# Kernel tuning notes

Hardware: AMD Instinct MI355X
Metric: run time of the kernel (lower is better)

The kernel has to match this reference:

```python
import jax, jax.numpy as jnp
import numpy as np

B, T, C = 8, 2048, 1024
HEAD = 64

def setup_inputs() -> dict:
    key = jax.random.key(0)
    k1, k2 = jax.random.split(key)
    x = jax.random.normal(k1, (B, T, C), dtype=jnp.float32)
    # nn.Linear(dim_embedding, head_size, bias=False) weight: [head_size, dim_embedding]
    W_k = jax.random.normal(k2, (HEAD, C), dtype=jnp.float32) * (C ** -0.5)
    return {"x": x, "W_k": W_k}

def reference(x, W_k):
    # Faithful to source: q, k, v are ALL computed with the `key` projection,
    # and the scale is C**-0.5 (embedding dim), as written in the torch code.
    Bx, Tx, Cx = x.shape
    k = jnp.einsum('btc,hc->bth', x, W_k)   # [B,T,HEAD]
    q = k
    v = k
    scale = Cx ** -0.5
    weight = jnp.einsum('bth,bsh->bts', q, k) * scale  # [B,T,T]
    causal = jnp.tril(jnp.ones((Tx, Tx), dtype=bool))
    weight = jnp.where(causal, weight, -jnp.inf)
    weight = jax.nn.softmax(weight, axis=-1)
    # dropout: eval-mode identity (p=0.2 at train time in the source)
    out = jnp.einsum('bts,bsh->bth', weight, v)  # [B,T,HEAD]
    return out
```

## Files before the change

kernel.cpp:

```cpp
#include <hip/hip_runtime.h>
#include <hip/hip_bf16.h>
#include <math.h>

#define SEQ   2048
#define CDIM  1024
#define HD    64
#define NROW  16384
#define CEXP 0.04508422002778112f

typedef float  f32x4  __attribute__((ext_vector_type(4)));
typedef __bf16 bf16x8 __attribute__((ext_vector_type(8)));
typedef int    i32x4  __attribute__((ext_vector_type(4)));

#define AS1 __attribute__((address_space(1)))
#define AS3 __attribute__((address_space(3)))

static __device__ __forceinline__ unsigned pk2(float a, float b) {
    unsigned ua = __builtin_bit_cast(unsigned, a);
    unsigned ub = __builtin_bit_cast(unsigned, b);
    ua += 0x7fffu + ((ua >> 16) & 1u);
    ub += 0x7fffu + ((ub >> 16) & 1u);
    return (ua >> 16) | (ub & 0xffff0000u);
}

static __device__ __forceinline__ bf16x8 cvt8(f32x4 lo, f32x4 hi) {
    i32x4 w = { (int)pk2(lo[0], lo[1]), (int)pk2(lo[2], lo[3]),
                (int)pk2(hi[0], hi[1]), (int)pk2(hi[2], hi[3]) };
    return __builtin_bit_cast(bf16x8, w);
}

__global__ __launch_bounds__(256) void wconv_kernel(const float* __restrict__ W,
                                                    unsigned* __restrict__ Wb) {
    const int i = blockIdx.x * 256 + threadIdx.x;
    float4 v = *(const float4*)(W + (size_t)i * 4);
    uint2 p = make_uint2(pk2(v.x, v.y), pk2(v.z, v.w));
    *(uint2*)(Wb + (size_t)i * 2) = p;
}

template<int S>
struct XProl {
    static __device__ __forceinline__ void run(f32x4 (&XA)[8], f32x4 (&XB)[8],
                                               unsigned long long xa) {
        constexpr int OFF = S * 128;
        asm volatile("global_load_dwordx4 %0, %2, off offset:%3\n\t"
                     "global_load_dwordx4 %1, %2, off offset:%4"
                     : "=&v"(XA[S]), "=&v"(XB[S])
                     : "v"(xa), "n"(OFF), "n"(OFF + 16)
                     : "memory");
        if constexpr (S + 1 < 8) XProl<S + 1>::run(XA, XB, xa);
    }
};

template<int T>
struct XLoop {
    static __device__ __forceinline__ void run(f32x4 (&XA)[8], f32x4 (&XB)[8],
                                               unsigned long long xa,
                                               const char* const (&wp)[4][2],
                                               f32x4 (&acc)[4]) {
        constexpr int WT = (T < 24) ? 14 : 2 * (31 - T);
        asm volatile("s_waitcnt vmcnt(%0)" :: "n"(WT) : "memory");
        __builtin_amdgcn_sched_barrier(0);
        bf16x8 A = cvt8(XA[T & 7], XB[T & 7]);
        #pragma unroll
        for (int nt = 0; nt < 4; ++nt) {
            bf16x8 B = *(const bf16x8*)(wp[nt][T & 1] + (T >> 1) * 128);
            acc[nt] = __builtin_amdgcn_mfma_f32_16x16x32_bf16(A, B, acc[nt], 0, 0, 0);
        }
        if constexpr (T < 24) {
            constexpr int OFF = (T + 8) * 128;
            asm volatile("global_load_dwordx4 %0, %2, off offset:%3\n\t"
                         "global_load_dwordx4 %1, %2, off offset:%4"
                         : "=&v"(XA[T & 7]), "=&v"(XB[T & 7])
                         : "v"(xa), "n"(OFF), "n"(OFF + 16)
                         : "memory");
        }
        if constexpr (T + 1 < 32) XLoop<T + 1>::run(XA, XB, xa, wp, acc);
    }
};

__global__ __launch_bounds__(256, 1) void proj_kernel(const float* __restrict__ x,
                                                      const unsigned short* __restrict__ Wb,
                                                      unsigned short* __restrict__ Ko,
                                                      uint2* __restrict__ KV2) {
    __shared__ __align__(16) char wlds[131072];

    const int tid = threadIdx.x;
    const int wid = tid >> 6, l = tid & 63, lm = l & 15, lg = l >> 4;
    const int bid = blockIdx.x;

    #pragma unroll
    for (int j = 0; j < 32; ++j) {
        int d = j * 4096 + tid * 16;
        int row = d >> 11, inner = d & 2047;
        int sin_ = inner ^ ((row & 7) << 4);
        const unsigned short* src = Wb + (size_t)row * CDIM + (sin_ >> 1);
        __builtin_amdgcn_global_load_lds((const AS1 void*)src,
                                         (AS3 void*)(wlds + j * 4096 + wid * 1024),
                                         16, 0, 0);
    }

    const int row = bid * 64 + wid * 16 + lm;
    unsigned long long xa =
        (unsigned long long)(const void*)(x + (size_t)row * CDIM + lg * 8);
    f32x4 XA[8], XB[8];
    XProl<0>::run(XA, XB, xa);

    asm volatile("s_waitcnt vmcnt(16)" ::: "memory");
    __builtin_amdgcn_sched_barrier(0);
    __builtin_amdgcn_s_barrier();
    __builtin_amdgcn_sched_barrier(0);

    const int hb = (lm >> 2) & 1;
    const int L  = ((lg ^ (lm & 3)) << 4);
    const char* wp[4][2];
    #pragma unroll
    for (int nt = 0; nt < 4; ++nt) {
        const char* base = wlds + (nt * 16 + lm) * 2048;
        wp[nt][0] = base + hb * 64 + L;
        wp[nt][1] = base + (1 - hb) * 64 + L;
    }

    f32x4 acc[4];
    acc[0] = acc[1] = acc[2] = acc[3] = (f32x4){0.f, 0.f, 0.f, 0.f};
    XLoop<0>::run(XA, XB, xa, wp, acc);

    const size_t m0r = (size_t)bid * 64 + wid * 16;
    #pragma unroll
    for (int nt = 0; nt < 4; ++nt)
        #pragma unroll
        for (int r = 0; r < 4; ++r)
            Ko[(m0r + lg * 4 + r) * HD + nt * 16 + lm] =
                (unsigned short)(pk2(acc[nt][r], 0.f) & 0xffffu);
    const size_t g = (size_t)bid * 4 + wid;
    #pragma unroll
    for (int nt = 0; nt < 4; ++nt)
        KV2[(g * 4 + nt) * 64 + l] =
            make_uint2(pk2(acc[nt][0], acc[nt][1]), pk2(acc[nt][2], acc[nt][3]));
}

struct KT { bf16x8 ka0, ka1; uint2 bv[4]; };

static __device__ __forceinline__ KT load_tile(const unsigned short* __restrict__ Kb,
                                               const uint2* __restrict__ KVb,
                                               int kt, int lm, int lg, int l) {
    KT t;
    const unsigned short* ar = Kb + (size_t)(kt * 16 + lm) * HD + lg * 8;
    t.ka0 = *(const bf16x8*)ar;
    t.ka1 = *(const bf16x8*)(ar + 32);
    const uint2* vp = KVb + (size_t)kt * 256 + l;
    #pragma unroll
    for (int nt = 0; nt < 4; ++nt) t.bv[nt] = vp[nt * 64];
    return t;
}

static __device__ __forceinline__ void proc_tile(const KT& t, bf16x8 bq0, bf16x8 bq1,
                                                 bool diag, int lm, int lg,
                                                 float& ls, f32x4 o[4]) {
    f32x4 s4 = (f32x4){0.f, 0.f, 0.f, 0.f};
    s4 = __builtin_amdgcn_mfma_f32_16x16x32_bf16(t.ka0, bq0, s4, 0, 0, 0);
    s4 = __builtin_amdgcn_mfma_f32_16x16x32_bf16(t.ka1, bq1, s4, 0, 0, 0);
    float s0 = s4[0], s1 = s4[1], s2 = s4[2], s3 = s4[3];
    if (diag) {
        const int kb = lg * 4;
        s0 = (kb + 0 > lm) ? -1e30f : s0;
        s1 = (kb + 1 > lm) ? -1e30f : s1;
        s2 = (kb + 2 > lm) ? -1e30f : s2;
        s3 = (kb + 3 > lm) ? -1e30f : s3;
    }
    float p0 = __builtin_amdgcn_exp2f(s0 * CEXP);
    float p1 = __builtin_amdgcn_exp2f(s1 * CEXP);
    float p2 = __builtin_amdgcn_exp2f(s2 * CEXP);
    float p3 = __builtin_amdgcn_exp2f(s3 * CEXP);
    ls += (p0 + p1) + (p2 + p3);
    bf16x8 pa = { (__bf16)p0, (__bf16)p1, (__bf16)p2, (__bf16)p3,
                  (__bf16)0.f, (__bf16)0.f, (__bf16)0.f, (__bf16)0.f };
    #pragma unroll
    for (int nt = 0; nt < 4; ++nt) {
        i32x4 vw = { (int)t.bv[nt].x, (int)t.bv[nt].y, 0, 0 };
        bf16x8 bvx = __builtin_bit_cast(bf16x8, vw);
        o[nt] = __builtin_amdgcn_mfma_f32_16x16x32_bf16(pa, bvx, o[nt], 0, 0, 0);
    }
}

static __device__ __forceinline__ void flash_qtile(const unsigned short* __restrict__ Kb,
                                                   const uint2* __restrict__ KVb,
                                                   int qt, int w, int lm, int lg, int l,
                                                   float& ls, f32x4 o[4]) {
    if (qt < w) return;
    const unsigned short* qr = Kb + (size_t)(qt * 16 + lm) * HD + lg * 8;
    bf16x8 bq0 = *(const bf16x8*)qr;
    bf16x8 bq1 = *(const bf16x8*)(qr + 32);
    const int last = qt - ((qt - w) & 3);
    KT A = load_tile(Kb, KVb, w, lm, lg, l);
    if (last == w) {
        proc_tile(A, bq0, bq1, last == qt, lm, lg, ls, o);
        return;
    }
    KT B = load_tile(Kb, KVb, w + 4, lm, lg, l);
    int kt = w;
    while (kt + 8 <= last) {
        KT C = load_tile(Kb, KVb, kt + 8, lm, lg, l);
        proc_tile(A, bq0, bq1, false, lm, lg, ls, o);
        A = B; B = C; kt += 4;
    }
    if (kt + 4 <= last) {
        proc_tile(A, bq0, bq1, false, lm, lg, ls, o);
        A = B; kt += 4;
    }
    proc_tile(A, bq0, bq1, last == qt, lm, lg, ls, o);
}

__global__ __launch_bounds__(256, 2) void attn_kernel(const unsigned short* __restrict__ K,
                                                      const uint2* __restrict__ KV2,
                                                      float* __restrict__ out) {
    __shared__ float oS[2][4][16][68];
    __shared__ float lS[2][4][16];
    const int tid = threadIdx.x;
    const int wid = tid >> 6, l = tid & 63, lm = l & 15, lg = l >> 4;
    const int b = blockIdx.x >> 6, i = blockIdx.x & 63;
    const unsigned short* Kb  = K   + (size_t)b * SEQ * HD;
    const uint2*          KVb = KV2 + (size_t)b * 128 * 256;

    #pragma unroll
    for (int s = 0; s < 2; ++s) {
        const int qt = s ? (127 - i) : i;
        float ls = 0.f;
        f32x4 o[4];
        o[0] = o[1] = o[2] = o[3] = (f32x4){0.f, 0.f, 0.f, 0.f};
        flash_qtile(Kb, KVb, qt, wid, lm, lg, l, ls, o);
        ls += __shfl_xor(ls, 16);
        ls += __shfl_xor(ls, 32);
        #pragma unroll
        for (int nt = 0; nt < 4; ++nt)
            #pragma unroll
            for (int r = 0; r < 4; ++r)
                oS[s][wid][lg * 4 + r][nt * 16 + lm] = o[nt][r];
        if (lg == 0) lS[s][wid][lm] = ls;
    }
    __syncthreads();

    const int slot = tid >> 7;
    const int row  = (tid >> 3) & 15;
    const int cg   = tid & 7;
    const int qt   = slot ? (127 - i) : i;
    float L = lS[slot][0][row] + lS[slot][1][row] + lS[slot][2][row] + lS[slot][3][row];
    const float inv = 1.f / L;
    f32x4 a0 = (f32x4){0.f, 0.f, 0.f, 0.f}, a1 = a0;
    #pragma unroll
    for (int w = 0; w < 4; ++w) {
        a0 += *(const f32x4*)&oS[slot][w][row][cg * 8];
        a1 += *(const f32x4*)&oS[slot][w][row][cg * 8 + 4];
    }
    float* op = out + ((size_t)b * SEQ + qt * 16 + row) * HD + cg * 8;
    *(f32x4*)op       = a0 * inv;
    *(f32x4*)(op + 4) = a1 * inv;
}

extern "C" void kernel_launch(void* const* d_in, const int* in_sizes, int n_in,
                              void* d_out, int out_size, void* d_ws, size_t ws_size,
                              hipStream_t stream) {
    const float* x  = (const float*)d_in[0];
    const float* Wk = (const float*)d_in[1];
    float* o        = (float*)d_out;
    unsigned short* Kp = (unsigned short*)d_ws;
    unsigned short* Wb = Kp + (size_t)NROW * HD;
    uint2* KV2 = (uint2*)(Wb + (size_t)HD * CDIM);

    wconv_kernel<<<64, 256, 0, stream>>>(Wk, (unsigned*)Wb);
    proj_kernel<<<256, 256, 0, stream>>>(x, Wb, Kp, KV2);
    attn_kernel<<<512, 256, 0, stream>>>(Kp, KV2, o);
}
```

Baseline: 47.90 us.

## Fuse weight conversion into projection and process four query tiles per attention block

Drops the separate W fp32-to-bf16 kernel: each projection block now loads fp32 W, converts it and writes it swizzled into LDS itself. K output stores are staged through LDS so they go out as 16-byte coalesced writes. The attention kernel now handles four query tiles per block (two from the front of the sequence, two from the back) and shares each loaded K/V tile across all four, halving the grid and cutting redundant K/V loads. The cost is more registers per wave (occupancy hint lowered to 1), redundant W conversion in every projection block, and a simpler, less deeply pipelined load loop in attention.

```diff
diff --git a/kernel.cpp b/kernel.cpp
--- a/kernel.cpp
+++ b/kernel.cpp
@@ -27,14 +27,6 @@
     i32x4 w = { (int)pk2(lo[0], lo[1]), (int)pk2(lo[2], lo[3]),
                 (int)pk2(hi[0], hi[1]), (int)pk2(hi[2], hi[3]) };
     return __builtin_bit_cast(bf16x8, w);
-}
-
-__global__ __launch_bounds__(256) void wconv_kernel(const float* __restrict__ W,
-                                                    unsigned* __restrict__ Wb) {
-    const int i = blockIdx.x * 256 + threadIdx.x;
-    float4 v = *(const float4*)(W + (size_t)i * 4);
-    uint2 p = make_uint2(pk2(v.x, v.y), pk2(v.z, v.w));
-    *(uint2*)(Wb + (size_t)i * 2) = p;
 }
 
 template<int S>
@@ -79,24 +71,28 @@
 };
 
 __global__ __launch_bounds__(256, 1) void proj_kernel(const float* __restrict__ x,
-                                                      const unsigned short* __restrict__ Wb,
+                                                      const float* __restrict__ W,
                                                       unsigned short* __restrict__ Ko,
                                                       uint2* __restrict__ KV2) {
     __shared__ __align__(16) char wlds[131072];
+    __shared__ __align__(16) unsigned short tb[4][16][64];
 
     const int tid = threadIdx.x;
     const int wid = tid >> 6, l = tid & 63, lm = l & 15, lg = l >> 4;
     const int bid = blockIdx.x;
 
     #pragma unroll
-    for (int j = 0; j < 32; ++j) {
-        int d = j * 4096 + tid * 16;
-        int row = d >> 11, inner = d & 2047;
-        int sin_ = inner ^ ((row & 7) << 4);
-        const unsigned short* src = Wb + (size_t)row * CDIM + (sin_ >> 1);
-        __builtin_amdgcn_global_load_lds((const AS1 void*)src,
-                                         (AS3 void*)(wlds + j * 4096 + wid * 1024),
-                                         16, 0, 0);
+    for (int c = 0; c < 4; ++c) {
+        float4 wv[16];
+        #pragma unroll
+        for (int j = 0; j < 16; ++j)
+            wv[j] = *(const float4*)(W + ((size_t)(c * 16 + j) * 256 + tid) * 4);
+        #pragma unroll
+        for (int j = 0; j < 16; ++j) {
+            const int r = c * 16 + j;
+            uint2 p = make_uint2(pk2(wv[j].x, wv[j].y), pk2(wv[j].z, wv[j].w));
+            *(uint2*)(wlds + r * 2048 + ((tid * 8) ^ ((r & 7) << 4))) = p;
+        }
     }
 
     const int row = bid * 64 + wid * 16 + lm;
@@ -105,7 +101,7 @@
     f32x4 XA[8], XB[8];
     XProl<0>::run(XA, XB, xa);
 
-    asm volatile("s_waitcnt vmcnt(16)" ::: "memory");
+    asm volatile("s_waitcnt lgkmcnt(0)" ::: "memory");
     __builtin_amdgcn_sched_barrier(0);
     __builtin_amdgcn_s_barrier();
     __builtin_amdgcn_sched_barrier(0);
@@ -124,13 +120,21 @@
     acc[0] = acc[1] = acc[2] = acc[3] = (f32x4){0.f, 0.f, 0.f, 0.f};
     XLoop<0>::run(XA, XB, xa, wp, acc);
 
+    #pragma unroll
+    for (int nt = 0; nt < 4; ++nt)
+        #pragma unroll
+        for (int r = 0; r < 4; ++r)
+            tb[wid][lg * 4 + r][nt * 16 + lm] =
+                (unsigned short)(pk2(acc[nt][r], 0.f) & 0xffffu);
     const size_t m0r = (size_t)bid * 64 + wid * 16;
-    #pragma unroll
-    for (int nt = 0; nt < 4; ++nt)
-        #pragma unroll
-        for (int r = 0; r < 4; ++r)
-            Ko[(m0r + lg * 4 + r) * HD + nt * 16 + lm] =
-                (unsigned short)(pk2(acc[nt][r], 0.f) & 0xffffu);
+    {
+        const char* tbase = (const char*)&tb[wid][0][0];
+        i32x4 v0 = *(const i32x4*)(tbase + l * 16);
+        i32x4 v1 = *(const i32x4*)(tbase + 1024 + l * 16);
+        char* kbase = (char*)(Ko + m0r * HD);
+        *(i32x4*)(kbase + l * 16)        = v0;
+        *(i32x4*)(kbase + 1024 + l * 16) = v1;
+    }
     const size_t g = (size_t)bid * 4 + wid;
     #pragma unroll
     for (int nt = 0; nt < 4; ++nt)
@@ -172,8 +176,8 @@
     float p2 = __builtin_amdgcn_exp2f(s2 * CEXP);
     float p3 = __builtin_amdgcn_exp2f(s3 * CEXP);
     ls += (p0 + p1) + (p2 + p3);
-    bf16x8 pa = { (__bf16)p0, (__bf16)p1, (__bf16)p2, (__bf16)p3,
-                  (__bf16)0.f, (__bf16)0.f, (__bf16)0.f, (__bf16)0.f };
+    i32x4 pw = { (int)pk2(p0, p1), (int)pk2(p2, p3), 0, 0 };
+    bf16x8 pa = __builtin_bit_cast(bf16x8, pw);
     #pragma unroll
     for (int nt = 0; nt < 4; ++nt) {
         i32x4 vw = { (int)t.bv[nt].x, (int)t.bv[nt].y, 0, 0 };
@@ -182,78 +186,79 @@
     }
 }
 
-static __device__ __forceinline__ void flash_qtile(const unsigned short* __restrict__ Kb,
-                                                   const uint2* __restrict__ KVb,
-                                                   int qt, int w, int lm, int lg, int l,
-                                                   float& ls, f32x4 o[4]) {
-    if (qt < w) return;
-    const unsigned short* qr = Kb + (size_t)(qt * 16 + lm) * HD + lg * 8;
-    bf16x8 bq0 = *(const bf16x8*)qr;
-    bf16x8 bq1 = *(const bf16x8*)(qr + 32);
-    const int last = qt - ((qt - w) & 3);
-    KT A = load_tile(Kb, KVb, w, lm, lg, l);
-    if (last == w) {
-        proc_tile(A, bq0, bq1, last == qt, lm, lg, ls, o);
-        return;
-    }
-    KT B = load_tile(Kb, KVb, w + 4, lm, lg, l);
-    int kt = w;
-    while (kt + 8 <= last) {
-        KT C = load_tile(Kb, KVb, kt + 8, lm, lg, l);
-        proc_tile(A, bq0, bq1, false, lm, lg, ls, o);
-        A = B; B = C; kt += 4;
-    }
-    if (kt + 4 <= last) {
-        proc_tile(A, bq0, bq1, false, lm, lg, ls, o);
-        A = B; kt += 4;
-    }
-    proc_tile(A, bq0, bq1, last == qt, lm, lg, ls, o);
-}
-
-__global__ __launch_bounds__(256, 2) void attn_kernel(const unsigned short* __restrict__ K,
+__global__ __launch_bounds__(256, 1) void attn_kernel(const unsigned short* __restrict__ K,
                                                       const uint2* __restrict__ KV2,
                                                       float* __restrict__ out) {
-    __shared__ float oS[2][4][16][68];
-    __shared__ float lS[2][4][16];
+    __shared__ float oS[4][4][16][68];
+    __shared__ float lS[4][4][16];
     const int tid = threadIdx.x;
     const int wid = tid >> 6, l = tid & 63, lm = l & 15, lg = l >> 4;
-    const int b = blockIdx.x >> 6, i = blockIdx.x & 63;
+    const int b = blockIdx.x >> 5, j = blockIdx.x & 31;
+    const int qts[4] = { 2 * j, 2 * j + 1, 126 - 2 * j, 127 - 2 * j };
     const unsigned short* Kb  = K   + (size_t)b * SEQ * HD;
     const uint2*          KVb = KV2 + (size_t)b * 128 * 256;
 
-    #pragma unroll
-    for (int s = 0; s < 2; ++s) {
-        const int qt = s ? (127 - i) : i;
-        float ls = 0.f;
-        f32x4 o[4];
-        o[0] = o[1] = o[2] = o[3] = (f32x4){0.f, 0.f, 0.f, 0.f};
-        flash_qtile(Kb, KVb, qt, wid, lm, lg, l, ls, o);
-        ls += __shfl_xor(ls, 16);
-        ls += __shfl_xor(ls, 32);
+    bf16x8 bq0[4], bq1[4];
+    #pragma unroll
+    for (int s = 0; s < 4; ++s) {
+        const unsigned short* qr = Kb + (size_t)(qts[s] * 16 + lm) * HD + lg * 8;
+        bq0[s] = *(const bf16x8*)qr;
+        bq1[s] = *(const bf16x8*)(qr + 32);
+    }
+
+    float ls[4] = { 0.f, 0.f, 0.f, 0.f };
+    f32x4 o[4][4];
+    #pragma unroll
+    for (int s = 0; s < 4; ++s)
+        #pragma unroll
+        for (int nt = 0; nt < 4; ++nt) o[s][nt] = (f32x4){0.f, 0.f, 0.f, 0.f};
+
+    auto process = [&](const KT& t, int kt) {
+        #pragma unroll
+        for (int s = 0; s < 4; ++s)
+            if (kt <= qts[s])
+                proc_tile(t, bq0[s], bq1[s], kt == qts[s], lm, lg, ls[s], o[s]);
+    };
+
+    const int qmax = qts[3];
+    KT A = load_tile(Kb, KVb, wid, lm, lg, l);
+    int kt = wid;
+    while (kt + 4 <= qmax) {
+        KT B = load_tile(Kb, KVb, kt + 4, lm, lg, l);
+        process(A, kt);
+        A = B; kt += 4;
+    }
+    process(A, kt);
+
+    #pragma unroll
+    for (int s = 0; s < 4; ++s) {
+        float lsum = ls[s];
+        lsum += __shfl_xor(lsum, 16);
+        lsum += __shfl_xor(lsum, 32);
         #pragma unroll
         for (int nt = 0; nt < 4; ++nt)
             #pragma unroll
             for (int r = 0; r < 4; ++r)
-                oS[s][wid][lg * 4 + r][nt * 16 + lm] = o[nt][r];
-        if (lg == 0) lS[s][wid][lm] = ls;
+                oS[s][wid][lg * 4 + r][nt * 16 + lm] = o[s][nt][r];
+        if (lg == 0) lS[s][wid][lm] = lsum;
     }
     __syncthreads();
 
-    const int slot = tid >> 7;
-    const int row  = (tid >> 3) & 15;
-    const int cg   = tid & 7;
-    const int qt   = slot ? (127 - i) : i;
-    float L = lS[slot][0][row] + lS[slot][1][row] + lS[slot][2][row] + lS[slot][3][row];
-    const float inv = 1.f / L;
-    f32x4 a0 = (f32x4){0.f, 0.f, 0.f, 0.f}, a1 = a0;
-    #pragma unroll
-    for (int w = 0; w < 4; ++w) {
-        a0 += *(const f32x4*)&oS[slot][w][row][cg * 8];
-        a1 += *(const f32x4*)&oS[slot][w][row][cg * 8 + 4];
-    }
-    float* op = out + ((size_t)b * SEQ + qt * 16 + row) * HD + cg * 8;
-    *(f32x4*)op       = a0 * inv;
-    *(f32x4*)(op + 4) = a1 * inv;
+    const int slot = wid;
+    const int row  = l >> 2;
+    const int cg   = l & 3;
+    const int qt   = (slot < 2) ? (2 * j + slot) : (126 - 2 * j + (slot - 2));
+    float Lsum = lS[slot][0][row] + lS[slot][1][row] + lS[slot][2][row] + lS[slot][3][row];
+    const float inv = 1.f / Lsum;
+    float* op = out + ((size_t)b * SEQ + qt * 16 + row) * HD + cg * 16;
+    #pragma unroll
+    for (int q4 = 0; q4 < 4; ++q4) {
+        f32x4 a = (f32x4){0.f, 0.f, 0.f, 0.f};
+        #pragma unroll
+        for (int w = 0; w < 4; ++w)
+            a += *(const f32x4*)&oS[slot][w][row][cg * 16 + q4 * 4];
+        *(f32x4*)(op + q4 * 4) = a * inv;
+    }
 }
 
 extern "C" void kernel_launch(void* const* d_in, const int* in_sizes, int n_in,
@@ -263,10 +268,8 @@
     const float* Wk = (const float*)d_in[1];
     float* o        = (float*)d_out;
     unsigned short* Kp = (unsigned short*)d_ws;
-    unsigned short* Wb = Kp + (size_t)NROW * HD;
-    uint2* KV2 = (uint2*)(Wb + (size_t)HD * CDIM);
-
-    wconv_kernel<<<64, 256, 0, stream>>>(Wk, (unsigned*)Wb);
-    proj_kernel<<<256, 256, 0, stream>>>(x, Wb, Kp, KV2);
-    attn_kernel<<<512, 256, 0, stream>>>(Kp, KV2, o);
-}
+    uint2* KV2 = (uint2*)(Kp + (size_t)NROW * HD);
+
+    proj_kernel<<<256, 256, 0, stream>>>(x, Wk, Kp, KV2);
+    attn_kernel<<<256, 256, 0, stream>>>(Kp, KV2, o);
+}
```

Result: faster. 38.74 us (median of 2 runs) (-19.1%).
